# Kernel optimization log

Hardware: AMD Instinct MI355X
Metric: run time of the kernel (lower is better)

## Reference

```python
import jax, jax.numpy as jnp
import numpy as np

B, E, LC, LE, D = 32, 8, 256, 512, 256   # batch, evi_num, claim_len, evidence_len, emb_dim
OUT, H = 128, 1                          # attention hidden dim, head_num
NEG = -1e18


def setup_inputs() -> dict:
    key = jax.random.key(0)
    ks = jax.random.split(key, 8)
    claim = jax.random.normal(ks[0], (B, E, LC, D), jnp.float32)
    evidence = jax.random.normal(ks[1], (B, E, LE, D), jnp.float32)
    claim_len_mask = jax.random.randint(ks[2], (B, E, 1, LC), 0, 2).astype(jnp.int32)
    evidence_len_mask = jax.random.randint(ks[3], (B, E, 1, LE), 0, 2).astype(jnp.int32)
    s2d = 1.0 / np.sqrt(2 * D)
    so = 1.0 / np.sqrt(OUT)
    W1 = jax.random.normal(ks[4], (2 * D, OUT), jnp.float32) * s2d  # torch W1.weight.T
    w2 = jax.random.normal(ks[5], (OUT, H), jnp.float32) * so
    W2 = jax.random.normal(ks[6], (2 * D, OUT), jnp.float32) * s2d
    w1 = jax.random.normal(ks[7], (OUT, H), jnp.float32) * so
    return {"claim": claim, "claim_len_mask": claim_len_mask,
            "evidence": evidence, "evidence_len_mask": evidence_len_mask,
            "W1": W1, "w2": w2, "W2": W2, "w1": w1}


def _pooled_attend(seq, seq_mask, pooled, W, w):
    # seq: (B,E,L,D), pooled: (B,E,1,D), W: (2D,OUT), w: (OUT,H)
    # cat([seq, pooled_expanded]) @ W  ==  seq @ W[:D] + pooled @ W[D:]  (broadcast)
    h = jnp.tanh(seq @ W[:D] + pooled @ W[D:])          # (B,E,L,OUT)
    att = h @ w                                          # (B,E,L,H)
    mask = jnp.swapaxes(seq_mask, -1, -2).astype(bool)   # (B,E,L,1), broadcast over H
    att = jnp.where(mask, att, NEG)
    scores = jax.nn.softmax(att, axis=-2)                # softmax over L
    out = jnp.einsum('belh,beld->behd', scores, seq)     # (B,E,H,D)
    return out.reshape(out.shape[0], out.shape[1], 1, -1)  # (B,E,1,H*D)


def reference(claim, claim_len_mask, evidence, evidence_len_mask, W1, w2, W2, w1):
    c_mean = jnp.mean(claim, axis=-2, keepdims=True)     # (B,E,1,D)
    e_hat = _pooled_attend(evidence, evidence_len_mask, c_mean, W1, w2)
    e_mean = jnp.mean(evidence, axis=-2, keepdims=True)  # (B,E,1,D)
    c_hat = _pooled_attend(claim, claim_len_mask, e_mean, W2, w1)
    return c_hat, e_hat
```

## Files before the change

### kernel.cpp

```cpp
#include <hip/hip_runtime.h>
#include <hip/hip_bf16.h>
#include <math.h>

#define BE   256
#define DIM  256
#define OUTD 128
#define LCL  256
#define LEV  512

#define NCH_EV 16
#define NCH_CL 8
#define NCHP   (NCH_EV + NCH_CL)
#define NBLK   (BE * NCHP)

typedef short  bf16x8  __attribute__((ext_vector_type(8)));
typedef float  floatx4 __attribute__((ext_vector_type(4)));

union BF1 { __hip_bfloat16 h; unsigned short u; };
union BF2 { __hip_bfloat162 h; unsigned int u; };

__device__ __forceinline__ float fast_tanh(float x) {
    float xc = fminf(fmaxf(x, -15.f), 15.f);
    float e = __expf(2.f * xc);
    return (e - 1.f) * __builtin_amdgcn_rcpf(e + 1.f);
}

__device__ __forceinline__ void gl_lds16(const float4* g, float4* l) {
    __builtin_amdgcn_global_load_lds(
        (const __attribute__((address_space(1))) unsigned int*)(const void*)g,
        (__attribute__((address_space(3))) unsigned int*)(void*)l,
        16, 0, 0);
}

__global__ __launch_bounds__(512) void k_meanbias(
    const float* __restrict__ claim, const float* __restrict__ evidence,
    const float* __restrict__ W1, const float* __restrict__ W2,
    const float* __restrict__ w2v, const float* __restrict__ w1v,
    float* __restrict__ bias_e, float* __restrict__ bias_c,
    unsigned short* __restrict__ WT1, unsigned short* __restrict__ WT2,
    float* __restrict__ Mval)
{
    const int bid = blockIdx.x;
    const int t = threadIdx.x;
    __shared__ float msum[8];
    if (bid >= BE) {
        const int side = bid - BE;
        const float* W = side ? W2 : W1;
        unsigned short* WT = side ? WT2 : WT1;
        for (int i = t; i < OUTD * DIM; i += 512) {
            const int d = i & (DIM - 1);
            const int n = i >> 8;
            BF1 c; c.h = __float2bfloat16(W[(size_t)d * OUTD + n]);
            WT[n * DIM + d] = c.u;
        }
        const float* wv_ = side ? w1v : w2v;
        float av = (t < OUTD) ? fabsf(wv_[t]) : 0.f;
#pragma unroll
        for (int off = 1; off < 64; off <<= 1) av += __shfl_xor(av, off, 64);
        if ((t & 63) == 0) msum[t >> 6] = av;
        __syncthreads();
        if (t == 0)
            Mval[side] = msum[0] + msum[1] + msum[2] + msum[3]
                       + msum[4] + msum[5] + msum[6] + msum[7];
        return;
    }
    const int pair = bid;
    const int d4 = t & 63, rg = t >> 6;
    __shared__ float4 smc[8][64];
    __shared__ float4 sme[8][64];
    __shared__ float mc[DIM], me[DIM];
    __shared__ float sb[2][2][OUTD];

    const float4* c4 = (const float4*)(claim + (size_t)pair * LCL * DIM);
    const float4* e4 = (const float4*)(evidence + (size_t)pair * LEV * DIM);
    float4 ac = make_float4(0.f, 0.f, 0.f, 0.f);
    float4 ae = make_float4(0.f, 0.f, 0.f, 0.f);
#pragma unroll 8
    for (int r = rg; r < LCL; r += 8) {
        const float4 v = c4[r * 64 + d4];
        ac.x += v.x; ac.y += v.y; ac.z += v.z; ac.w += v.w;
    }
#pragma unroll 8
    for (int r = rg; r < LEV; r += 8) {
        const float4 v = e4[r * 64 + d4];
        ae.x += v.x; ae.y += v.y; ae.z += v.z; ae.w += v.w;
    }
    smc[rg][d4] = ac; sme[rg][d4] = ae;
    __syncthreads();
    if (t < 64) {
        float4 s = make_float4(0.f, 0.f, 0.f, 0.f);
#pragma unroll
        for (int j = 0; j < 8; ++j) {
            const float4 v = smc[j][t];
            s.x += v.x; s.y += v.y; s.z += v.z; s.w += v.w;
        }
        ((float4*)mc)[t] = make_float4(s.x * (1.f / LCL), s.y * (1.f / LCL),
                                       s.z * (1.f / LCL), s.w * (1.f / LCL));
    } else if (t < 128) {
        const int u = t - 64;
        float4 s = make_float4(0.f, 0.f, 0.f, 0.f);
#pragma unroll
        for (int j = 0; j < 8; ++j) {
            const float4 v = sme[j][u];
            s.x += v.x; s.y += v.y; s.z += v.z; s.w += v.w;
        }
        ((float4*)me)[u] = make_float4(s.x * (1.f / LEV), s.y * (1.f / LEV),
                                       s.z * (1.f / LEV), s.w * (1.f / LEV));
    }
    __syncthreads();
    const int side = t >> 8, o = t & 127, dh = (t >> 7) & 1;
    const float* W = side ? W2 : W1;
    const float* m = side ? me : mc;
    float s = 0.f;
#pragma unroll 8
    for (int i = 0; i < 128; ++i) {
        const int d = dh * 128 + i;
        s += m[d] * W[(size_t)(DIM + d) * OUTD + o];
    }
    sb[side][dh][o] = s;
    __syncthreads();
    if (t < 256) {
        const int sd = t >> 7, oo = t & 127;
        const float bv = sb[sd][0][oo] + sb[sd][1][oo];
        (sd ? bias_c : bias_e)[pair * OUTD + oo] = bv;
    }
}

__global__ __launch_bounds__(256, 2) void k_main(
    const float* __restrict__ claim, const float* __restrict__ evidence,
    const unsigned short* __restrict__ WT1, const unsigned short* __restrict__ WT2,
    const float* __restrict__ w2v, const float* __restrict__ w1v,
    const float* __restrict__ bias_e, const float* __restrict__ bias_c,
    const int* __restrict__ emask, const int* __restrict__ cmask,
    const float* __restrict__ Mval,
    float* __restrict__ O_part, float* __restrict__ l_part)
{
    constexpr int TR  = 32;
    constexpr int SR4 = 65;
    __shared__ float4 sA4[TR * SR4];
    __shared__ float sred[4][TR];

    const int bid = blockIdx.x;
    const int pair = bid / NCHP;
    const int c = bid - pair * NCHP;
    const bool is_ev = c < NCH_EV;
    const int chunk = is_ev ? c : c - NCH_EV;
    const float* __restrict__ seq  = is_ev ? evidence : claim;
    const unsigned short* __restrict__ WT = is_ev ? WT1 : WT2;
    const float* __restrict__ wvec = is_ev ? w2v : w1v;
    const float* __restrict__ bias = is_ev ? bias_e : bias_c;
    const int*   __restrict__ mask = is_ev ? emask : cmask;
    const int L = is_ev ? LEV : LCL;
    const float M = Mval[is_ev ? 0 : 1];

    const int t = threadIdx.x;
    const int lane = t & 63;
    const int wv = t >> 6;
    const int q = lane >> 4, c16 = lane & 15;

    float bc[2], wc[2];
#pragma unroll
    for (int ct = 0; ct < 2; ++ct) {
        const int col = wv * 32 + ct * 16 + c16;
        bc[ct] = bias[pair * OUTD + col];
        wc[ct] = wvec[col];
    }
    bf16x8 breg[16];
#pragma unroll
    for (int ks = 0; ks < 8; ++ks)
#pragma unroll
        for (int ct = 0; ct < 2; ++ct)
            breg[ks * 2 + ct] = *(const bf16x8*)(
                WT + (size_t)(wv * 32 + ct * 16 + c16) * DIM + ks * 32 + q * 8);

    const float4* base = (const float4*)(seq + ((size_t)pair * L + chunk * TR) * DIM);
#pragma unroll
    for (int j = 0; j < 8; ++j) {
        const int row = wv * 8 + j;
        gl_lds16(base + row * 64 + lane, &sA4[row * SR4]);
    }
    const int mk = mask[pair * L + chunk * TR + (lane & 31)];
    __syncthreads();

    floatx4 acc[2][2];
    acc[0][0] = (floatx4){0.f, 0.f, 0.f, 0.f};
    acc[0][1] = (floatx4){0.f, 0.f, 0.f, 0.f};
    acc[1][0] = (floatx4){0.f, 0.f, 0.f, 0.f};
    acc[1][1] = (floatx4){0.f, 0.f, 0.f, 0.f};
#pragma unroll
    for (int ks = 0; ks < 8; ++ks) {
#pragma unroll
        for (int ra = 0; ra < 2; ++ra) {
            const float4 lo = sA4[(ra * 16 + c16) * SR4 + ks * 8 + q * 2];
            const float4 hi = sA4[(ra * 16 + c16) * SR4 + ks * 8 + q * 2 + 1];
            union { bf16x8 v; BF2 p[4]; } ua;
            ua.p[0].h = __float22bfloat162_rn(make_float2(lo.x, lo.y));
            ua.p[1].h = __float22bfloat162_rn(make_float2(lo.z, lo.w));
            ua.p[2].h = __float22bfloat162_rn(make_float2(hi.x, hi.y));
            ua.p[3].h = __float22bfloat162_rn(make_float2(hi.z, hi.w));
#pragma unroll
            for (int ct = 0; ct < 2; ++ct)
                acc[ra][ct] = __builtin_amdgcn_mfma_f32_16x16x32_bf16(
                    ua.v, breg[ks * 2 + ct], acc[ra][ct], 0, 0, 0);
        }
    }

#pragma unroll
    for (int ra = 0; ra < 2; ++ra) {
#pragma unroll
        for (int reg = 0; reg < 4; ++reg) {
            float s = fast_tanh(acc[ra][0][reg] + bc[0]) * wc[0]
                    + fast_tanh(acc[ra][1][reg] + bc[1]) * wc[1];
#pragma unroll
            for (int off = 1; off < 16; off <<= 1) s += __shfl_xor(s, off, 64);
            if (c16 == 0)
                sred[wv][ra * 16 + q * 4 + reg] = s;
        }
    }
    __syncthreads();

    const int r31 = lane & 31;
    const float a = sred[0][r31] + sred[1][r31] + sred[2][r31] + sred[3][r31];
    const float e = mk ? __expf(a - M) : 0.f;
    float sl = e;
#pragma unroll
    for (int off = 1; off < 32; off <<= 1) sl += __shfl_xor(sl, off, 64);

    float4 Oac = make_float4(0.f, 0.f, 0.f, 0.f);
#pragma unroll
    for (int r = 0; r < 8; ++r) {
        const int rw = wv * 8 + r;
        const float pl = __shfl(e, rw, 64);
        const float4 v = sA4[rw * SR4 + lane];
        Oac.x += pl * v.x; Oac.y += pl * v.y; Oac.z += pl * v.z; Oac.w += pl * v.w;
    }

    __syncthreads();
    ((float4*)sA4)[t] = Oac;
    __syncthreads();
    if (t < 64) {
        float4 s = make_float4(0.f, 0.f, 0.f, 0.f);
#pragma unroll
        for (int j = 0; j < 4; ++j) {
            const float4 v = ((float4*)sA4)[j * 64 + t];
            s.x += v.x; s.y += v.y; s.z += v.z; s.w += v.w;
        }
        ((float4*)(O_part + (size_t)bid * DIM))[t] = s;
    }
    if (t == 0) l_part[bid] = sl;
}

__global__ __launch_bounds__(64) void k_combine(
    const float* __restrict__ O_part, const float* __restrict__ l_part,
    float* __restrict__ out)
{
    const int bid = blockIdx.x;
    const int t = threadIdx.x;
    const bool is_ev = (bid & 1) == 0;
    const int pair = bid >> 1;
    const int base = pair * NCHP + (is_ev ? 0 : NCH_EV);
    const int NC = is_ev ? NCH_EV : NCH_CL;
    float* __restrict__ outp = is_ev ? out + (size_t)BE * DIM : out;

    float4 s = make_float4(0.f, 0.f, 0.f, 0.f);
    float l = 0.f;
    for (int i = 0; i < NC; ++i) {
        const float4 v = ((const float4*)(O_part + (size_t)(base + i) * DIM))[t];
        s.x += v.x; s.y += v.y; s.z += v.z; s.w += v.w;
        l += l_part[base + i];
    }
    const float inv = 1.f / l;
    ((float4*)(outp + (size_t)pair * DIM))[t] =
        make_float4(s.x * inv, s.y * inv, s.z * inv, s.w * inv);
}

extern "C" void kernel_launch(void* const* d_in, const int* in_sizes, int n_in,
                              void* d_out, int out_size, void* d_ws, size_t ws_size,
                              hipStream_t stream) {
    const float* claim    = (const float*)d_in[0];
    const int*   cmask    = (const int*)  d_in[1];
    const float* evidence = (const float*)d_in[2];
    const int*   emask    = (const int*)  d_in[3];
    const float* W1       = (const float*)d_in[4];
    const float* w2       = (const float*)d_in[5];
    const float* W2       = (const float*)d_in[6];
    const float* w1       = (const float*)d_in[7];
    float* out = (float*)d_out;

    float* ws = (float*)d_ws;
    float* bias_e = ws;
    float* bias_c = bias_e + BE * OUTD;
    float* O_part = bias_c + BE * OUTD;
    float* l_part = O_part + (size_t)NBLK * DIM;
    float* Mval   = l_part + NBLK;
    unsigned short* WT1 = (unsigned short*)(Mval + 2);
    unsigned short* WT2 = WT1 + OUTD * DIM;

    k_meanbias<<<BE + 2, 512, 0, stream>>>(claim, evidence, W1, W2, w2, w1,
                                           bias_e, bias_c, WT1, WT2, Mval);
    k_main<<<NBLK, 256, 0, stream>>>(claim, evidence, WT1, WT2, w2, w1,
                                     bias_e, bias_c, emask, cmask, Mval,
                                     O_part, l_part);
    k_combine<<<2 * BE, 64, 0, stream>>>(O_part, l_part, out);
}
```

Before: 330.8 us.

## Split mean reduction into chunked partial-sum kernel plus reduce-and-bias kernel

The mean pooling over claim and evidence sequences moves out of a 256-block kernel into a new kernel with one block per 32-row chunk, giving 6144 blocks that each write a partial sum. A second kernel adds up the partials, then computes the pooled bias and the bf16 weight transpose as before. The goal is to raise memory-level parallelism for the full read of both inputs, which the old kernel did with few blocks. The cost is an extra launch and a scratch buffer, which reuses the O_part region later written by the main kernel.

```diff
diff --git a/kernel.cpp b/kernel.cpp
--- a/kernel.cpp
+++ b/kernel.cpp
@@ -25,6 +25,10 @@
     return (e - 1.f) * __builtin_amdgcn_rcpf(e + 1.f);
 }
 
+__device__ __forceinline__ float4 f4add(float4 a, float4 b) {
+    return make_float4(a.x + b.x, a.y + b.y, a.z + b.z, a.w + b.w);
+}
+
 __device__ __forceinline__ void gl_lds16(const float4* g, float4* l) {
     __builtin_amdgcn_global_load_lds(
         (const __attribute__((address_space(1))) unsigned int*)(const void*)g,
@@ -32,8 +36,44 @@
         16, 0, 0);
 }
 
-__global__ __launch_bounds__(512) void k_meanbias(
+__global__ __launch_bounds__(256, 4) void k_meanpart(
     const float* __restrict__ claim, const float* __restrict__ evidence,
+    float* __restrict__ partial)
+{
+    const int bid = blockIdx.x;
+    const int pair = bid / NCHP;
+    const int c = bid - pair * NCHP;
+    const bool is_ev = c < NCH_EV;
+    const int chunk = is_ev ? c : c - NCH_EV;
+    const float* __restrict__ seq = is_ev ? evidence : claim;
+    const int L = is_ev ? LEV : LCL;
+
+    const int t = threadIdx.x;
+    const int d4 = t & 63, wv = t >> 6;
+    const float4* base = (const float4*)(seq + ((size_t)pair * L + chunk * 32) * DIM);
+
+    float4 v0 = base[(wv * 8 + 0) * 64 + d4];
+    float4 v1 = base[(wv * 8 + 1) * 64 + d4];
+    float4 v2 = base[(wv * 8 + 2) * 64 + d4];
+    float4 v3 = base[(wv * 8 + 3) * 64 + d4];
+    float4 v4 = base[(wv * 8 + 4) * 64 + d4];
+    float4 v5 = base[(wv * 8 + 5) * 64 + d4];
+    float4 v6 = base[(wv * 8 + 6) * 64 + d4];
+    float4 v7 = base[(wv * 8 + 7) * 64 + d4];
+    const float4 s = f4add(f4add(f4add(v0, v1), f4add(v2, v3)),
+                           f4add(f4add(v4, v5), f4add(v6, v7)));
+
+    __shared__ float4 sm[4][64];
+    sm[wv][d4] = s;
+    __syncthreads();
+    if (t < 64) {
+        const float4 r = f4add(f4add(sm[0][t], sm[1][t]), f4add(sm[2][t], sm[3][t]));
+        ((float4*)(partial + (size_t)bid * DIM))[t] = r;
+    }
+}
+
+__global__ __launch_bounds__(512) void k_redbias(
+    const float* __restrict__ partial,
     const float* __restrict__ W1, const float* __restrict__ W2,
     const float* __restrict__ w2v, const float* __restrict__ w1v,
     float* __restrict__ bias_e, float* __restrict__ bias_c,
@@ -65,47 +105,20 @@
         return;
     }
     const int pair = bid;
-    const int d4 = t & 63, rg = t >> 6;
-    __shared__ float4 smc[8][64];
-    __shared__ float4 sme[8][64];
     __shared__ float mc[DIM], me[DIM];
     __shared__ float sb[2][2][OUTD];
-
-    const float4* c4 = (const float4*)(claim + (size_t)pair * LCL * DIM);
-    const float4* e4 = (const float4*)(evidence + (size_t)pair * LEV * DIM);
-    float4 ac = make_float4(0.f, 0.f, 0.f, 0.f);
-    float4 ae = make_float4(0.f, 0.f, 0.f, 0.f);
-#pragma unroll 8
-    for (int r = rg; r < LCL; r += 8) {
-        const float4 v = c4[r * 64 + d4];
-        ac.x += v.x; ac.y += v.y; ac.z += v.z; ac.w += v.w;
-    }
-#pragma unroll 8
-    for (int r = rg; r < LEV; r += 8) {
-        const float4 v = e4[r * 64 + d4];
-        ae.x += v.x; ae.y += v.y; ae.z += v.z; ae.w += v.w;
-    }
-    smc[rg][d4] = ac; sme[rg][d4] = ae;
-    __syncthreads();
-    if (t < 64) {
-        float4 s = make_float4(0.f, 0.f, 0.f, 0.f);
-#pragma unroll
-        for (int j = 0; j < 8; ++j) {
-            const float4 v = smc[j][t];
-            s.x += v.x; s.y += v.y; s.z += v.z; s.w += v.w;
-        }
-        ((float4*)mc)[t] = make_float4(s.x * (1.f / LCL), s.y * (1.f / LCL),
-                                       s.z * (1.f / LCL), s.w * (1.f / LCL));
-    } else if (t < 128) {
-        const int u = t - 64;
-        float4 s = make_float4(0.f, 0.f, 0.f, 0.f);
-#pragma unroll
-        for (int j = 0; j < 8; ++j) {
-            const float4 v = sme[j][u];
-            s.x += v.x; s.y += v.y; s.z += v.z; s.w += v.w;
-        }
-        ((float4*)me)[u] = make_float4(s.x * (1.f / LEV), s.y * (1.f / LEV),
-                                       s.z * (1.f / LEV), s.w * (1.f / LEV));
+    const float* pb = partial + (size_t)pair * NCHP * DIM;
+    if (t < 256) {
+        float s = 0.f;
+#pragma unroll
+        for (int j = 0; j < NCH_CL; ++j) s += pb[(NCH_EV + j) * DIM + t];
+        mc[t] = s * (1.f / LCL);
+    } else {
+        const int t2 = t - 256;
+        float s = 0.f;
+#pragma unroll
+        for (int j = 0; j < NCH_EV; ++j) s += pb[j * DIM + t2];
+        me[t2] = s * (1.f / LEV);
     }
     __syncthreads();
     const int side = t >> 8, o = t & 127, dh = (t >> 7) & 1;
@@ -290,16 +303,17 @@
     float* ws = (float*)d_ws;
     float* bias_e = ws;
     float* bias_c = bias_e + BE * OUTD;
-    float* O_part = bias_c + BE * OUTD;
-    float* l_part = O_part + (size_t)NBLK * DIM;
+    float* buf    = bias_c + BE * OUTD;
+    float* l_part = buf + (size_t)NBLK * DIM;
     float* Mval   = l_part + NBLK;
     unsigned short* WT1 = (unsigned short*)(Mval + 2);
     unsigned short* WT2 = WT1 + OUTD * DIM;
 
-    k_meanbias<<<BE + 2, 512, 0, stream>>>(claim, evidence, W1, W2, w2, w1,
-                                           bias_e, bias_c, WT1, WT2, Mval);
+    k_meanpart<<<NBLK, 256, 0, stream>>>(claim, evidence, buf);
+    k_redbias<<<BE + 2, 512, 0, stream>>>(buf, W1, W2, w2, w1,
+                                          bias_e, bias_c, WT1, WT2, Mval);
     k_main<<<NBLK, 256, 0, stream>>>(claim, evidence, WT1, WT2, w2, w1,
                                      bias_e, bias_c, emask, cmask, Mval,
-                                     O_part, l_part);
-    k_combine<<<2 * BE, 64, 0, stream>>>(O_part, l_part, out);
-}
+                                     buf, l_part);
+    k_combine<<<2 * BE, 64, 0, stream>>>(buf, l_part, out);
+}
```

Measured after the change: 339.7 us. 1.03x slower.
